# Optimization experiments

Measured on AMD Instinct MI355X. Metric: run time of the kernel, lower is better.

Reference implementation:

```python
import jax, jax.numpy as jnp
import numpy as np

B, H, E, K = 8192, 1024, 8, 2


def setup_inputs() -> dict:
    key = jax.random.key(0)
    k1, k2, k3 = jax.random.split(key, 3)
    x = jax.random.normal(k1, (B, H), dtype=jnp.float32)
    gate_w = jax.random.normal(k2, (H, E), dtype=jnp.float32) / np.sqrt(H)
    expert_w = jax.random.normal(k3, (E, H, H), dtype=jnp.float32) / np.sqrt(H)
    return {"x": x, "gate_w": gate_w, "expert_w": expert_w}


def reference(x, gate_w, expert_w):
    # Gate: logits over experts, top-k routing, softmax over the k selected logits
    logits = x @ gate_w                               # [B, E]
    top_w, top_idx = jax.lax.top_k(logits, K)         # [B, K]
    top_w = jax.nn.softmax(top_w, axis=-1)            # softmax over the K selected
    # Combine weights scattered back to [B, E]; zero for unselected experts
    combine = jnp.zeros((x.shape[0], expert_w.shape[0]), dtype=x.dtype)
    combine = combine.at[jnp.arange(x.shape[0])[:, None], top_idx].add(top_w)
    # Expert GEMMs (dense dispatch reference: every expert on every token,
    # masked/weighted by combine; mathematically identical to gather/scatter)
    expert_out = jnp.einsum('bh,eho->beo', x, expert_w)   # [B, E, H]
    out = jnp.einsum('be,beo->bo', combine, expert_out)   # [B, H]
    return out
```

## Files before the change

### kernel.cpp

```cpp
#include <hip/hip_runtime.h>
#include <hip/hip_bf16.h>
#include <stdint.h>

#define B_TOK 8192
#define H_DIM 1024
#define E_NUM 8
#define NSLOT (2 * B_TOK)

typedef __attribute__((ext_vector_type(8))) short short8;
typedef __attribute__((ext_vector_type(4))) float floatx4;

__device__ __forceinline__ unsigned short f32_to_bf16_rne(float f) {
  union { float f; uint32_t u; } v; v.f = f;
  uint32_t u = v.u;
  uint32_t r = u + 0x7FFFu + ((u >> 16) & 1u);
  return (unsigned short)(r >> 16);
}
__device__ __forceinline__ float bf16_to_f32(unsigned short s) {
  union { uint32_t u; float f; } v; v.u = ((uint32_t)s) << 16;
  return v.f;
}

__global__ __launch_bounds__(256) void prep_kernel(const float* __restrict__ x,
                                                   const float* __restrict__ gw,
                                                   const float* __restrict__ ew,
                                                   unsigned short* __restrict__ xb,
                                                   unsigned short* __restrict__ wt,
                                                   int2* __restrict__ re,
                                                   float2* __restrict__ rw) {
  __shared__ float smem[E_NUM * 1028];
  int bid = blockIdx.x;
  int tid = threadIdx.x;
  if (bid < 2048) {
    float (*tile)[65] = (float(*)[65])smem;
    int e = bid >> 8;
    int n0 = ((bid >> 4) & 15) * 64, k0 = (bid & 15) * 64;
    const float* wb = ew + ((size_t)e * H_DIM + k0) * H_DIM + n0;
    unsigned short* wtb = wt + ((size_t)e * H_DIM + n0) * H_DIM + k0;
    int rr = tid >> 4, c4 = tid & 15;
#pragma unroll
    for (int j = 0; j < 4; ++j) {
      int r = rr + j * 16;
      float4 v = *(const float4*)(wb + (size_t)r * H_DIM + c4 * 4);
      tile[c4 * 4 + 0][r] = v.x;
      tile[c4 * 4 + 1][r] = v.y;
      tile[c4 * 4 + 2][r] = v.z;
      tile[c4 * 4 + 3][r] = v.w;
    }
    __syncthreads();
#pragma unroll
    for (int j = 0; j < 4; ++j) {
      int nr = rr + j * 16;
      float4 v = *(const float4*)&tile[nr][c4 * 4];
      ushort4 o;
      o.x = f32_to_bf16_rne(v.x); o.y = f32_to_bf16_rne(v.y);
      o.z = f32_to_bf16_rne(v.z); o.w = f32_to_bf16_rne(v.w);
      *(ushort4*)(wtb + (size_t)nr * H_DIM + c4 * 4) = o;
    }
  } else {
    int rb = bid - 2048;
    float (*gws)[1028] = (float(*)[1028])smem;
#pragma unroll
    for (int it = 0; it < 8; ++it) {
      int i4 = it * 256 + tid;
      float4 v = ((const float4*)gw)[i4];
      int h = i4 >> 1, e0 = (i4 & 1) * 4;
      gws[e0 + 0][h] = v.x;
      gws[e0 + 1][h] = v.y;
      gws[e0 + 2][h] = v.z;
      gws[e0 + 3][h] = v.w;
    }
    __syncthreads();
    int wid = tid >> 6, lane = tid & 63;
    int b0 = rb * 16 + wid * 4;
    const float4* xr0 = (const float4*)(x + (size_t)(b0 + 0) * H_DIM);
    const float4* xr1 = (const float4*)(x + (size_t)(b0 + 1) * H_DIM);
    const float4* xr2 = (const float4*)(x + (size_t)(b0 + 2) * H_DIM);
    const float4* xr3 = (const float4*)(x + (size_t)(b0 + 3) * H_DIM);
    const float4* xr[4] = {xr0, xr1, xr2, xr3};
    float acc[4][E_NUM];
#pragma unroll
    for (int t = 0; t < 4; ++t)
#pragma unroll
      for (int e = 0; e < E_NUM; e++) acc[t][e] = 0.f;
#pragma unroll
    for (int it = 0; it < 4; ++it) {
      int c4 = it * 64 + lane;
      int h = c4 * 4;
      float4 g[E_NUM];
#pragma unroll
      for (int e = 0; e < E_NUM; e++) g[e] = *(const float4*)&gws[e][h];
#pragma unroll
      for (int t = 0; t < 4; ++t) {
        float4 v = xr[t][c4];
        ushort4 o;
        o.x = f32_to_bf16_rne(v.x); o.y = f32_to_bf16_rne(v.y);
        o.z = f32_to_bf16_rne(v.z); o.w = f32_to_bf16_rne(v.w);
        ((ushort4*)(xb + (size_t)(b0 + t) * H_DIM))[c4] = o;
#pragma unroll
        for (int e = 0; e < E_NUM; e++)
          acc[t][e] += v.x * g[e].x + v.y * g[e].y + v.z * g[e].z + v.w * g[e].w;
      }
    }
#pragma unroll
    for (int t = 0; t < 4; ++t) {
#pragma unroll
      for (int e = 0; e < E_NUM; e++) {
#pragma unroll
        for (int off = 32; off; off >>= 1) acc[t][e] += __shfl_xor(acc[t][e], off, 64);
      }
      if (lane == 0) {
        int b = b0 + t;
        int e0 = 0; float v0 = acc[t][0];
#pragma unroll
        for (int e = 1; e < E_NUM; e++) if (acc[t][e] > v0) { v0 = acc[t][e]; e0 = e; }
        int e1 = -1; float v1 = -1e30f;
#pragma unroll
        for (int e = 0; e < E_NUM; e++) if (e != e0 && acc[t][e] > v1) { v1 = acc[t][e]; e1 = e; }
        float s = expf(v1 - v0);
        float w0 = 1.0f / (1.0f + s);
        re[b] = make_int2(e0, e1);
        rw[b] = make_float2(w0, s * w0);
      }
    }
  }
}

__global__ __launch_bounds__(1024) void compact_kernel(const int2* __restrict__ re,
                                                       int* __restrict__ slot_tok,
                                                       int* __restrict__ yslot,
                                                       int* __restrict__ ebase,
                                                       int* __restrict__ ecnt) {
  __shared__ int wcnt[8][16];
  __shared__ int bless[16];
  int e = blockIdx.x;
  int tid = threadIdx.x, wid = tid >> 6, lane = tid & 63;
  int cless = 0;
  int flag[8];
  unsigned long long mm[8];
#pragma unroll
  for (int it = 0; it < 8; ++it) {
    int2 ee = re[it * 1024 + tid];
    cless += (ee.x < e) + (ee.y < e);
    bool f0 = (ee.x == e), f1 = (ee.y == e);
    flag[it] = f0 ? 1 : (f1 ? 2 : 0);
    mm[it] = __ballot(f0 || f1);
    if (lane == 0) wcnt[it][wid] = __popcll(mm[it]);
  }
#pragma unroll
  for (int off = 32; off; off >>= 1) cless += __shfl_xor(cless, off, 64);
  if (lane == 0) bless[wid] = cless;
  __syncthreads();
  int base = 0;
#pragma unroll
  for (int i = 0; i < 16; ++i) base += bless[i];
  int run = 0;
#pragma unroll
  for (int it = 0; it < 8; ++it) {
    int wbase = 0, total = 0;
#pragma unroll
    for (int i = 0; i < 16; ++i) { int v = wcnt[it][i]; if (i < wid) wbase += v; total += v; }
    if (flag[it]) {
      int pre = __popcll(mm[it] & ((1ull << lane) - 1ull));
      int s = base + run + wbase + pre;
      int t = it * 1024 + tid;
      slot_tok[s] = t;
      yslot[2 * t + (flag[it] == 1 ? 0 : 1)] = s;
    }
    run += total;
  }
  if (tid == 0) { ebase[e] = base; ecnt[e] = run; }
}

__device__ __forceinline__ void async_ld16(const void* g, void* l) {
  __builtin_amdgcn_global_load_lds((const __attribute__((address_space(1))) void*)g,
                                   (__attribute__((address_space(3))) void*)l, 16, 0, 0);
}

__global__ __launch_bounds__(256, 2) void moe_gemm_kernel(
    const unsigned short* __restrict__ xb,
    const unsigned short* __restrict__ wt,
    const int* __restrict__ ebase,
    const int* __restrict__ ecnt,
    const int* __restrict__ slot_tok,
    unsigned short* __restrict__ y) {
  int e = blockIdx.z;
  int c = ecnt[e];
  int m0 = blockIdx.y * 128;
  if (m0 >= c) return;
  int base = ebase[e];
  int n0 = blockIdx.x * 256;

  __shared__ __align__(16) unsigned short As[128 * 64];
  __shared__ __align__(16) unsigned short Bs[256 * 64];

  int tid = threadIdx.x, wid = tid >> 6, lane = tid & 63;
  int rloc = lane >> 3;
  int cl = lane & 7;
  const int* st = slot_tok + base;

  const unsigned short* gA[4];
  const unsigned short* gB[8];
  unsigned short* lA[4];
  unsigned short* lB[8];
#pragma unroll
  for (int j = 0; j < 4; ++j) {
    int rl = wid * 32 + j * 8 + rloc;
    int g = (cl ^ (rl & 7)) * 8;
    int ra = min(m0 + rl, c - 1);
    gA[j] = xb + (size_t)st[ra] * H_DIM + g;
    lA[j] = As + (wid * 32 + j * 8) * 64;
  }
#pragma unroll
  for (int j = 0; j < 8; ++j) {
    int rl = wid * 64 + j * 8 + rloc;
    int g = (cl ^ (rl & 7)) * 8;
    gB[j] = wt + ((size_t)e * H_DIM + n0 + rl) * H_DIM + g;
    lB[j] = Bs + (wid * 64 + j * 8) * 64;
  }

  floatx4 acc[4][8];
#pragma unroll
  for (int a = 0; a < 4; ++a)
#pragma unroll
    for (int b = 0; b < 8; ++b)
#pragma unroll
      for (int q = 0; q < 4; ++q) acc[a][b][q] = 0.0f;

  int wm = (wid >> 1) * 64, wn = (wid & 1) * 128;
  int mr = lane & 15, kg = lane >> 4;
  int sw = mr & 7;

  for (int ks = 0; ks < 16; ++ks) {
    __syncthreads();
#pragma unroll
    for (int j = 0; j < 4; ++j) async_ld16(gA[j], lA[j]);
#pragma unroll
    for (int j = 0; j < 8; ++j) async_ld16(gB[j], lB[j]);
#pragma unroll
    for (int j = 0; j < 4; ++j) gA[j] += 64;
#pragma unroll
    for (int j = 0; j < 8; ++j) gB[j] += 64;
    __syncthreads();
#pragma unroll
    for (int kk = 0; kk < 2; ++kk) {
      int cb = ((kk * 4 + kg) ^ sw) * 8;
      short8 af[4], bfr[8];
#pragma unroll
      for (int t = 0; t < 4; ++t)
        af[t] = *(const short8*)(const void*)(As + (wm + t * 16 + mr) * 64 + cb);
#pragma unroll
      for (int u = 0; u < 8; ++u)
        bfr[u] = *(const short8*)(const void*)(Bs + (wn + u * 16 + mr) * 64 + cb);
#pragma unroll
      for (int tm = 0; tm < 4; ++tm)
#pragma unroll
        for (int tn = 0; tn < 8; ++tn)
          acc[tm][tn] = __builtin_amdgcn_mfma_f32_16x16x32_bf16(af[tm], bfr[tn], acc[tm][tn], 0, 0, 0);
    }
  }

#pragma unroll
  for (int tm = 0; tm < 4; ++tm) {
#pragma unroll
    for (int q = 0; q < 4; ++q) {
      int r = m0 + wm + tm * 16 + kg * 4 + q;
      if (r < c) {
        unsigned short* yrow = y + (size_t)(base + r) * H_DIM + n0 + wn + mr;
#pragma unroll
        for (int tn = 0; tn < 8; ++tn) yrow[tn * 16] = f32_to_bf16_rne(acc[tm][tn][q]);
      }
    }
  }
}

__global__ __launch_bounds__(256) void combine_kernel(const unsigned short* __restrict__ y,
                                                      const int* __restrict__ yslot,
                                                      const float2* __restrict__ rw,
                                                      float* __restrict__ out) {
  int wid = threadIdx.x >> 6, lane = threadIdx.x & 63;
  int t = blockIdx.x * 4 + wid;
  int s0 = yslot[2 * t], s1 = yslot[2 * t + 1];
  float2 w = rw[t];
  const ushort4* y0 = (const ushort4*)(y + (size_t)s0 * H_DIM);
  const ushort4* y1 = (const ushort4*)(y + (size_t)s1 * H_DIM);
  float4* o = (float4*)(out + (size_t)t * H_DIM);
  ushort4 a[4], b[4];
#pragma unroll
  for (int j = 0; j < 4; ++j) {
    int i = j * 64 + lane;
    a[j] = y0[i];
    b[j] = y1[i];
  }
#pragma unroll
  for (int j = 0; j < 4; ++j) {
    int i = j * 64 + lane;
    float4 r;
    r.x = w.x * bf16_to_f32(a[j].x) + w.y * bf16_to_f32(b[j].x);
    r.y = w.x * bf16_to_f32(a[j].y) + w.y * bf16_to_f32(b[j].y);
    r.z = w.x * bf16_to_f32(a[j].z) + w.y * bf16_to_f32(b[j].z);
    r.w = w.x * bf16_to_f32(a[j].w) + w.y * bf16_to_f32(b[j].w);
    o[i] = r;
  }
}

extern "C" void kernel_launch(void* const* d_in, const int* in_sizes, int n_in,
                              void* d_out, int out_size, void* d_ws, size_t ws_size,
                              hipStream_t stream) {
  const float* x  = (const float*)d_in[0];
  const float* gw = (const float*)d_in[1];
  const float* ew = (const float*)d_in[2];
  float* out = (float*)d_out;

  char* ws = (char*)d_ws;
  unsigned short* xb = (unsigned short*)ws;
  unsigned short* wt = (unsigned short*)(ws + (size_t)16 * 1024 * 1024);
  unsigned short* y  = (unsigned short*)(ws + (size_t)32 * 1024 * 1024);
  char* p = ws + (size_t)64 * 1024 * 1024;
  int2*   re       = (int2*)p;
  float2* rw       = (float2*)(p + (64 << 10));
  int*    slot_tok = (int*)(p + (128 << 10));
  int*    yslot    = (int*)(p + (192 << 10));
  int*    ebase    = (int*)(p + (256 << 10));
  int*    ecnt     = (int*)(p + (256 << 10) + 64);

  prep_kernel<<<2560, 256, 0, stream>>>(x, gw, ew, xb, wt, re, rw);
  compact_kernel<<<E_NUM, 1024, 0, stream>>>(re, slot_tok, yslot, ebase, ecnt);
  moe_gemm_kernel<<<dim3(4, 32, E_NUM), 256, 0, stream>>>(
      xb, wt, ebase, ecnt, slot_tok, y);
  combine_kernel<<<B_TOK / 4, 256, 0, stream>>>(y, yslot, rw, out);
}
```

Before: 182.1 us.

## Shrink MoE GEMM tile to 128x128 with grouped block order and 32-bit offsets

The expert GEMM tile is reduced from 128x256 to 128x128, which halves per-wave accumulators, and occupancy is raised to 4 blocks per CU. Blocks are remapped so groups of 8 M-tiles share the same N tile, aiming for better L2 reuse of weight and activation rows. Global addresses become 32-bit byte offsets and the wave id is made uniform via readfirstlane to cut address registers. The trade-off is less data reuse per tile and more blocks, with twice as many A-tile loads overall.

```diff
diff --git a/kernel.cpp b/kernel.cpp
--- a/kernel.cpp
+++ b/kernel.cpp
@@ -177,7 +177,7 @@
                                    (__attribute__((address_space(3))) void*)l, 16, 0, 0);
 }
 
-__global__ __launch_bounds__(256, 2) void moe_gemm_kernel(
+__global__ __launch_bounds__(256, 4) void moe_gemm_kernel(
     const unsigned short* __restrict__ xb,
     const unsigned short* __restrict__ wt,
     const int* __restrict__ ebase,
@@ -186,77 +186,74 @@
     unsigned short* __restrict__ y) {
   int e = blockIdx.z;
   int c = ecnt[e];
-  int m0 = blockIdx.y * 128;
+  int m_idx = ((blockIdx.y >> 3) << 3) + blockIdx.x;
+  int n_idx = blockIdx.y & 7;
+  int m0 = m_idx * 128;
   if (m0 >= c) return;
   int base = ebase[e];
-  int n0 = blockIdx.x * 256;
+  int n0 = n_idx * 128;
 
   __shared__ __align__(16) unsigned short As[128 * 64];
-  __shared__ __align__(16) unsigned short Bs[256 * 64];
-
-  int tid = threadIdx.x, wid = tid >> 6, lane = tid & 63;
+  __shared__ __align__(16) unsigned short Bs[128 * 64];
+
+  int tid = threadIdx.x, lane = tid & 63;
+  int widu = __builtin_amdgcn_readfirstlane(tid >> 6);
   int rloc = lane >> 3;
   int cl = lane & 7;
   const int* st = slot_tok + base;
 
-  const unsigned short* gA[4];
-  const unsigned short* gB[8];
+  const char* xbB = (const char*)xb;
+  const char* wtB = (const char*)wt;
+  uint32_t oA[4], oB[4];
   unsigned short* lA[4];
-  unsigned short* lB[8];
+  unsigned short* lB[4];
 #pragma unroll
   for (int j = 0; j < 4; ++j) {
-    int rl = wid * 32 + j * 8 + rloc;
+    int rl = widu * 32 + j * 8 + rloc;
     int g = (cl ^ (rl & 7)) * 8;
     int ra = min(m0 + rl, c - 1);
-    gA[j] = xb + (size_t)st[ra] * H_DIM + g;
-    lA[j] = As + (wid * 32 + j * 8) * 64;
-  }
-#pragma unroll
-  for (int j = 0; j < 8; ++j) {
-    int rl = wid * 64 + j * 8 + rloc;
-    int g = (cl ^ (rl & 7)) * 8;
-    gB[j] = wt + ((size_t)e * H_DIM + n0 + rl) * H_DIM + g;
-    lB[j] = Bs + (wid * 64 + j * 8) * 64;
-  }
-
-  floatx4 acc[4][8];
+    oA[j] = ((uint32_t)st[ra] * H_DIM + g) * 2;
+    oB[j] = ((uint32_t)(e * H_DIM + n0 + rl) * H_DIM + g) * 2;
+    lA[j] = As + (widu * 32 + j * 8) * 64;
+    lB[j] = Bs + (widu * 32 + j * 8) * 64;
+  }
+
+  floatx4 acc[4][4];
 #pragma unroll
   for (int a = 0; a < 4; ++a)
 #pragma unroll
-    for (int b = 0; b < 8; ++b)
+    for (int b = 0; b < 4; ++b)
 #pragma unroll
       for (int q = 0; q < 4; ++q) acc[a][b][q] = 0.0f;
 
-  int wm = (wid >> 1) * 64, wn = (wid & 1) * 128;
+  int wm = (widu >> 1) * 64, wn = (widu & 1) * 64;
   int mr = lane & 15, kg = lane >> 4;
   int sw = mr & 7;
 
   for (int ks = 0; ks < 16; ++ks) {
     __syncthreads();
 #pragma unroll
-    for (int j = 0; j < 4; ++j) async_ld16(gA[j], lA[j]);
-#pragma unroll
-    for (int j = 0; j < 8; ++j) async_ld16(gB[j], lB[j]);
-#pragma unroll
-    for (int j = 0; j < 4; ++j) gA[j] += 64;
-#pragma unroll
-    for (int j = 0; j < 8; ++j) gB[j] += 64;
+    for (int j = 0; j < 4; ++j) {
+      async_ld16(xbB + oA[j], lA[j]);
+      async_ld16(wtB + oB[j], lB[j]);
+    }
+#pragma unroll
+    for (int j = 0; j < 4; ++j) { oA[j] += 128; oB[j] += 128; }
     __syncthreads();
 #pragma unroll
     for (int kk = 0; kk < 2; ++kk) {
       int cb = ((kk * 4 + kg) ^ sw) * 8;
-      short8 af[4], bfr[8];
+      short8 af[4];
 #pragma unroll
       for (int t = 0; t < 4; ++t)
         af[t] = *(const short8*)(const void*)(As + (wm + t * 16 + mr) * 64 + cb);
 #pragma unroll
-      for (int u = 0; u < 8; ++u)
-        bfr[u] = *(const short8*)(const void*)(Bs + (wn + u * 16 + mr) * 64 + cb);
-#pragma unroll
-      for (int tm = 0; tm < 4; ++tm)
-#pragma unroll
-        for (int tn = 0; tn < 8; ++tn)
-          acc[tm][tn] = __builtin_amdgcn_mfma_f32_16x16x32_bf16(af[tm], bfr[tn], acc[tm][tn], 0, 0, 0);
+      for (int tn = 0; tn < 4; ++tn) {
+        short8 bfr = *(const short8*)(const void*)(Bs + (wn + tn * 16 + mr) * 64 + cb);
+#pragma unroll
+        for (int tm = 0; tm < 4; ++tm)
+          acc[tm][tn] = __builtin_amdgcn_mfma_f32_16x16x32_bf16(af[tm], bfr, acc[tm][tn], 0, 0, 0);
+      }
     }
   }
 
@@ -268,7 +265,7 @@
       if (r < c) {
         unsigned short* yrow = y + (size_t)(base + r) * H_DIM + n0 + wn + mr;
 #pragma unroll
-        for (int tn = 0; tn < 8; ++tn) yrow[tn * 16] = f32_to_bf16_rne(acc[tm][tn][q]);
+        for (int tn = 0; tn < 4; ++tn) yrow[tn * 16] = f32_to_bf16_rne(acc[tm][tn][q]);
       }
     }
   }
@@ -326,7 +323,7 @@
 
   prep_kernel<<<2560, 256, 0, stream>>>(x, gw, ew, xb, wt, re, rw);
   compact_kernel<<<E_NUM, 1024, 0, stream>>>(re, slot_tok, yslot, ebase, ecnt);
-  moe_gemm_kernel<<<dim3(4, 32, E_NUM), 256, 0, stream>>>(
+  moe_gemm_kernel<<<dim3(8, 64, E_NUM), 256, 0, stream>>>(
       xb, wt, ebase, ecnt, slot_tok, y);
   combine_kernel<<<B_TOK / 4, 256, 0, stream>>>(y, yslot, rw, out);
 }
```

Result: faster. 174.6 us (-4.1%).
